# Kernel optimization log

Measured on AMD Instinct MI355X. Metric: run time of the kernel, lower is better.

## Reference

```python
import jax, jax.numpy as jnp
import numpy as np
import math

H = 16        # num heads
D = 64        # head dim
HID = 1024    # hidden size
MULT = 2      # GIN MLP multiplier
FRAC = 0.1    # top_k fraction of available predecessors
THR = 0.2     # threshold value
BASE = 10000.0  # rope base
CHUNK = 32    # query-row chunk for max aggregator
NEG = -1e30


def _rope(x, pos):
    # x: (b, H, S, D); pos: (b, S) int
    d = x.shape[-1]
    inv = 1.0 / (BASE ** (jnp.arange(0, d, 2, dtype=jnp.float32) / d))
    ang = pos.astype(jnp.float32)[..., None] * inv            # (b, S, d//2)
    cos = jnp.concatenate([jnp.cos(ang)] * 2, -1)[:, None]    # (b, 1, S, d)
    sin = jnp.concatenate([jnp.sin(ang)] * 2, -1)[:, None]
    x1, x2 = jnp.split(x, 2, axis=-1)
    return x * cos + jnp.concatenate([-x2, x1], -1) * sin


def _scaled_topk_causal(adj):
    # faithful vectorization of scaled_topk_causal_4d: per query row i, keep
    # top max(1, ceil(FRAC*i)) of the (threshold-filtered) strict predecessors.
    S = adj.shape[-1]
    j = jnp.arange(S)
    strict = j[None, :] < j[:, None]                           # (S, S) j < i
    # torch: filtered = a[:, :i] * (a >= thr)  -> below-threshold become 0
    filtered = jnp.where(strict, jnp.where(adj >= THR, adj, 0.0), NEG)
    order = jnp.argsort(-filtered, axis=-1)                    # descending, stable
    rank = jnp.argsort(order, axis=-1)                         # inverse permutation
    k = jnp.maximum(1, jnp.ceil(FRAC * jnp.arange(S, dtype=jnp.float32))).astype(jnp.int32)
    k = k.at[0].set(0)                                         # row 0 has no predecessors
    return ((rank < k[None, None, :, None]) & strict).astype(adj.dtype)


def reference(hidden_states, Wq, Wk, Wv, Wo, W1, W2, eps, position_ids):
    b, S, _ = hidden_states.shape
    q = (hidden_states @ Wq).reshape(b, S, H, D).transpose(0, 2, 1, 3)
    kk = (hidden_states @ Wk).reshape(b, S, H, D).transpose(0, 2, 1, 3)
    v = (hidden_states @ Wv).reshape(b, S, H, D).transpose(0, 2, 1, 3)
    q = _rope(q, position_ids)
    kk = _rope(kk, position_ids)
    scores = jnp.einsum('bhid,bhjd->bhij', q, kk) / math.sqrt(D)
    adj = _scaled_topk_causal(scores)                          # binary (b,H,S,S)
    deg = adj.sum(-1)                                          # (b,H,S)
    denom = jnp.maximum(deg, 1.0)[..., None]
    s_agg = jnp.einsum('bhij,bhjd->bhid', adj, v)              # sum
    m_agg = s_agg / denom                                      # mean
    var = jnp.maximum(jnp.einsum('bhij,bhjd->bhid', adj, v * v) / denom - m_agg ** 2, 0.0)
    # max aggregator: masked max over selected predecessors, chunked over rows
    nc = S // CHUNK
    adj_c = jnp.moveaxis(adj.reshape(b, H, nc, CHUNK, S), 2, 0)  # (nc,b,H,C,S)
    mx = jax.lax.map(
        lambda ac: jnp.max(jnp.where(ac[..., None] > 0, v[:, :, None, :, :], NEG), axis=-2),
        adj_c)                                                 # (nc,b,H,C,D)
    mx = jnp.moveaxis(mx, 0, 2).reshape(b, H, S, D)
    mx = jnp.where(deg[..., None] > 0, mx, 0.0)
    comb = jnp.concatenate([s_agg, m_agg, mx, var], -1)        # (b,H,S,4D)
    h1 = jax.nn.silu(jnp.einsum('bhsf,hfm->bhsm', comb, W1))   # per-head GIN MLP
    head_out = jnp.einsum('bhsm,hmd->bhsd', h1, W2) + eps * v  # epsilon-scaled residual
    return head_out.transpose(0, 2, 1, 3).reshape(b, S, H * D) @ Wo


def setup_inputs() -> dict:
    key = jax.random.key(0)
    ks = jax.random.split(key, 8)
    b, S = 1, 1024
    sc = 0.02
    return {
        'hidden_states': jax.random.normal(ks[0], (b, S, HID), jnp.float32),
        'Wq': jax.random.normal(ks[1], (HID, H * D), jnp.float32) * sc,
        'Wk': jax.random.normal(ks[2], (HID, H * D), jnp.float32) * sc,
        'Wv': jax.random.normal(ks[3], (HID, H * D), jnp.float32) * sc,
        'Wo': jax.random.normal(ks[4], (H * D, HID), jnp.float32) * sc,
        'W1': jax.random.normal(ks[5], (H, 4 * D, MULT * D), jnp.float32) * sc,
        'W2': jax.random.normal(ks[6], (H, MULT * D, D), jnp.float32) * sc,
        'eps': jnp.asarray(0.1, jnp.float32),
        'position_ids': jnp.arange(S, dtype=jnp.int32)[None, :],
    }
```

## Files before the change

### kernel.cpp

```cpp
#include <hip/hip_runtime.h>
#include <math.h>

#define NEGF  -1e30f
#define TAU   1e-6f

static __device__ __forceinline__ int imin(int a, int b) { return a < b ? a : b; }

static __device__ __forceinline__ void fma44(float A[4][4], const float4 xa, const float4 yb) {
  A[0][0] += xa.x * yb.x; A[0][1] += xa.x * yb.y; A[0][2] += xa.x * yb.z; A[0][3] += xa.x * yb.w;
  A[1][0] += xa.y * yb.x; A[1][1] += xa.y * yb.y; A[1][2] += xa.y * yb.z; A[1][3] += xa.y * yb.w;
  A[2][0] += xa.z * yb.x; A[2][1] += xa.z * yb.y; A[2][2] += xa.z * yb.z; A[2][3] += xa.z * yb.w;
  A[3][0] += xa.w * yb.x; A[3][1] += xa.w * yb.y; A[3][2] += xa.w * yb.z; A[3][3] += xa.w * yb.w;
}

static __device__ __forceinline__ void fold44(float T[4][4], float A[4][4]) {
#pragma unroll
  for (int e = 0; e < 4; ++e)
#pragma unroll
    for (int f = 0; f < 4; ++f) { T[e][f] = __fadd_rn(T[e][f], A[e][f]); A[e][f] = 0.0f; }
}

template <int MODE>
__global__ __launch_bounds__(256) void gemm64(
    const float* __restrict__ A, const float* __restrict__ B, float* __restrict__ C,
    const float* __restrict__ R, const float* __restrict__ eps_p,
    int M, int N, int K, int lda, int ldb, int ldc,
    long sA, long sB, long sC)
{
  const int z = blockIdx.z;
  A += (long)z * sA;
  B += (long)z * sB;
  float* Cf = C + (long)z * sC;
  const float* Rz = (MODE == 2) ? (R + (long)z * sC) : nullptr;

  const int bm = blockIdx.x * 64;
  const int bn = blockIdx.y * 64;
  const int tid = threadIdx.x;
  const int r0 = (tid >> 4) * 4;
  const int c0 = (tid & 15) * 4;

  __shared__ float As[16][68];
  __shared__ float Bs[16][64];

  float acc[4][4] = {};

  const int ar = tid >> 2;
  const int ac = (tid & 3) * 4;
  const int br = tid >> 4;
  const int bc = (tid & 15) * 4;

  for (int kt = 0; kt < K; kt += 16) {
    float4 av = *(const float4*)(A + (long)(bm + ar) * lda + kt + ac);
    float4 bv = *(const float4*)(B + (long)(kt + br) * ldb + bn + bc);
    As[ac + 0][ar] = av.x;
    As[ac + 1][ar] = av.y;
    As[ac + 2][ar] = av.z;
    As[ac + 3][ar] = av.w;
    *(float4*)&Bs[br][bc] = bv;
    __syncthreads();
#pragma unroll
    for (int kk = 0; kk < 16; ++kk) {
      const float4 xa = *(const float4*)&As[kk][r0];
      const float4 yb = *(const float4*)&Bs[kk][c0];
      fma44(acc, xa, yb);
    }
    __syncthreads();
  }

  const float ev = (MODE == 2) ? eps_p[0] : 0.0f;
#pragma unroll
  for (int e = 0; e < 4; ++e)
#pragma unroll
    for (int f = 0; f < 4; ++f) {
      const int r = bm + r0 + e;
      const int c = bn + c0 + f;
      float x = acc[e][f];
      if (MODE == 1) x = x / (1.0f + expf(-x));
      if (MODE == 2) x += ev * Rz[(long)r * ldc + c];
      Cf[(long)r * ldc + c] = x;
    }
}

__global__ __launch_bounds__(256) void gemm_qkv_s48(
    const float* __restrict__ A,
    const float* __restrict__ Wq, const float* __restrict__ Wk, const float* __restrict__ Wv,
    float* __restrict__ part)
{
  const int z = blockIdx.z;
  const int mat = z % 3;
  const int panel = z / 3;
  const float* B = (mat == 0) ? Wq : (mat == 1) ? Wk : Wv;
  float* P = part + ((long)(mat * 3 + panel) << 20);

  const int k0 = panel * 384;
  const int k1 = (panel == 2) ? 1024 : (k0 + 384);

  const int bm = blockIdx.x * 64;
  const int bn = blockIdx.y * 128;
  const int tid = threadIdx.x;
  const int r0 = (tid >> 4) * 4;
  const int c0 = (tid & 15) * 4;

  __shared__ float As[2][16][68];
  __shared__ float Bs[2][16][132];

  float aL[4][4] = {}, aR[4][4] = {};

  const int ar = tid >> 2;
  const int ac = (tid & 3) * 4;
  const int br = tid >> 4;
  const int bc = (tid & 15) * 4;

  {
    float4 av = *(const float4*)(A + (long)(bm + ar) * 1024 + k0 + ac);
    float4 b0 = *(const float4*)(B + (long)(k0 + br) * 1024 + bn + bc);
    float4 b1 = *(const float4*)(B + (long)(k0 + br) * 1024 + bn + bc + 64);
    As[0][ac + 0][ar] = av.x; As[0][ac + 1][ar] = av.y;
    As[0][ac + 2][ar] = av.z; As[0][ac + 3][ar] = av.w;
    *(float4*)&Bs[0][br][bc] = b0;
    *(float4*)&Bs[0][br][bc + 64] = b1;
  }
  __syncthreads();

  int cur = 0;
  for (int kt = k0; kt < k1; kt += 16) {
    const bool more = (kt + 16 < k1);
    float4 avn, b0n, b1n;
    if (more) {
      avn = *(const float4*)(A + (long)(bm + ar) * 1024 + kt + 16 + ac);
      b0n = *(const float4*)(B + (long)(kt + 16 + br) * 1024 + bn + bc);
      b1n = *(const float4*)(B + (long)(kt + 16 + br) * 1024 + bn + bc + 64);
    }
#pragma unroll
    for (int kk = 0; kk < 16; ++kk) {
      const float4 xa = *(const float4*)&As[cur][kk][r0];
      const float4 y0 = *(const float4*)&Bs[cur][kk][c0];
      const float4 y1 = *(const float4*)&Bs[cur][kk][64 + c0];
      fma44(aL, xa, y0);
      fma44(aR, xa, y1);
    }
    if (more) {
      const int nxt = cur ^ 1;
      As[nxt][ac + 0][ar] = avn.x; As[nxt][ac + 1][ar] = avn.y;
      As[nxt][ac + 2][ar] = avn.z; As[nxt][ac + 3][ar] = avn.w;
      *(float4*)&Bs[nxt][br][bc] = b0n;
      *(float4*)&Bs[nxt][br][bc + 64] = b1n;
      __syncthreads();
      cur = nxt;
    }
  }

#pragma unroll
  for (int e = 0; e < 4; ++e) {
    float* prow = P + (long)(bm + r0 + e) * 1024 + bn;
#pragma unroll
    for (int f = 0; f < 4; ++f) {
      prow[c0 + f]      = aL[e][f];
      prow[64 + c0 + f] = aR[e][f];
    }
  }
}

__global__ __launch_bounds__(256) void combine_qkv(
    const float4* __restrict__ part, float4* __restrict__ dst)
{
  const int idx = blockIdx.x * 256 + threadIdx.x;
  const int mat = idx >> 18;
  const int w = idx & 0x3FFFF;
  const long b = (long)(mat * 3) << 18;
  const float4 s0 = part[b + w];
  const float4 s1 = part[b + (1L << 18) + w];
  const float4 s2 = part[b + (2L << 18) + w];
  float4 r;
  r.x = __fadd_rn(__fadd_rn(s0.x, s1.x), s2.x);
  r.y = __fadd_rn(__fadd_rn(s0.y, s1.y), s2.y);
  r.z = __fadd_rn(__fadd_rn(s0.z, s1.z), s2.z);
  r.w = __fadd_rn(__fadd_rn(s0.w, s1.w), s2.w);
  dst[idx] = r;
}

__global__ __launch_bounds__(256) void combine_out(
    const float4* __restrict__ p, float4* __restrict__ dst)
{
  const int idx = blockIdx.x * 256 + threadIdx.x;
  const float4 a = p[idx];
  const float4 b = p[idx + (1 << 18)];
  float4 r;
  r.x = __fadd_rn(a.x, b.x);
  r.y = __fadd_rn(a.y, b.y);
  r.z = __fadd_rn(a.z, b.z);
  r.w = __fadd_rn(a.w, b.w);
  dst[idx] = r;
}

__global__ __launch_bounds__(256) void gemm_qkv64(
    const float* __restrict__ A,
    const float* __restrict__ Wq, const float* __restrict__ Wk, const float* __restrict__ Wv,
    float* __restrict__ qo, float* __restrict__ ko, float* __restrict__ vo)
{
  const int z = blockIdx.z;
  const float* B = (z == 0) ? Wq : (z == 1) ? Wk : Wv;
  float* C = (z == 0) ? qo : (z == 1) ? ko : vo;

  const int bm = blockIdx.x * 64;
  const int bn = blockIdx.y * 64;
  const int tid = threadIdx.x;
  const int r0 = (tid >> 4) * 4;
  const int c0 = (tid & 15) * 4;

  __shared__ float As[2][32][68];
  __shared__ float Bs[2][32][64];

  float acc[4][4] = {};
  float tot[4][4] = {};

  const int ar = tid >> 2;
  const int ac = (tid & 3) * 8;
  const int br = tid >> 3;
  const int bc = (tid & 7) * 8;

  {
    float4 a0 = *(const float4*)(A + (long)(bm + ar) * 1024 + ac);
    float4 a1 = *(const float4*)(A + (long)(bm + ar) * 1024 + ac + 4);
    float4 b0 = *(const float4*)(B + (long)br * 1024 + bn + bc);
    float4 b1 = *(const float4*)(B + (long)br * 1024 + bn + bc + 4);
    As[0][ac + 0][ar] = a0.x; As[0][ac + 1][ar] = a0.y;
    As[0][ac + 2][ar] = a0.z; As[0][ac + 3][ar] = a0.w;
    As[0][ac + 4][ar] = a1.x; As[0][ac + 5][ar] = a1.y;
    As[0][ac + 6][ar] = a1.z; As[0][ac + 7][ar] = a1.w;
    *(float4*)&Bs[0][br][bc] = b0;
    *(float4*)&Bs[0][br][bc + 4] = b1;
  }
  __syncthreads();

  int cur = 0;
  for (int kt = 0; kt < 1024; kt += 32) {
    const bool more = (kt + 32 < 1024);
    float4 a0n, a1n, b0n, b1n;
    if (more) {
      a0n = *(const float4*)(A + (long)(bm + ar) * 1024 + kt + 32 + ac);
      a1n = *(const float4*)(A + (long)(bm + ar) * 1024 + kt + 32 + ac + 4);
      b0n = *(const float4*)(B + (long)(kt + 32 + br) * 1024 + bn + bc);
      b1n = *(const float4*)(B + (long)(kt + 32 + br) * 1024 + bn + bc + 4);
    }
    if (kt == 384 || kt == 768) {
      fold44(tot, acc);
    }
#pragma unroll
    for (int kk = 0; kk < 32; ++kk) {
      const float4 xa = *(const float4*)&As[cur][kk][r0];
      const float4 yb = *(const float4*)&Bs[cur][kk][c0];
      fma44(acc, xa, yb);
    }
    if (more) {
      const int nxt = cur ^ 1;
      As[nxt][ac + 0][ar] = a0n.x; As[nxt][ac + 1][ar] = a0n.y;
      As[nxt][ac + 2][ar] = a0n.z; As[nxt][ac + 3][ar] = a0n.w;
      As[nxt][ac + 4][ar] = a1n.x; As[nxt][ac + 5][ar] = a1n.y;
      As[nxt][ac + 6][ar] = a1n.z; As[nxt][ac + 7][ar] = a1n.w;
      *(float4*)&Bs[nxt][br][bc] = b0n;
      *(float4*)&Bs[nxt][br][bc + 4] = b1n;
      __syncthreads();
      cur = nxt;
    }
  }

#pragma unroll
  for (int e = 0; e < 4; ++e)
#pragma unroll
    for (int f = 0; f < 4; ++f)
      C[(long)(bm + r0 + e) * 1024 + bn + c0 + f] = __fadd_rn(tot[e][f], acc[e][f]);
}

__global__ __launch_bounds__(256) void rope_table(
    const int* __restrict__ pos_ids, float2* __restrict__ tab)
{
  const int g = blockIdx.x * 256 + threadIdx.x;
  const int t = g & 31;
  const int s = g >> 5;

  const float e = (float)(2 * t) / 64.0f;
  const float p32 = (float)pow(10000.0, (double)e);
  const float inv = __fdiv_rn(1.0f, p32);
  const float posf = (float)pos_ids[s];
  const float ang = __fmul_rn(posf, inv);
  tab[g] = make_float2((float)cos((double)ang), (float)sin((double)ang));
}

__global__ __launch_bounds__(256) void rope_apply(float* __restrict__ q,
                                                  float* __restrict__ kb,
                                                  const float2* __restrict__ tab)
{
  const int g = blockIdx.x * blockDim.x + threadIdx.x;
  const int t = g & 31;
  const int h = (g >> 5) & 15;
  const int s = (g >> 9) & 1023;
  const int buf = g >> 19;
  float* p = buf ? kb : q;

  const float2 cs = tab[s * 32 + t];
  const float c  = cs.x;
  const float sn = cs.y;

  const int base = s * 1024 + h * 64;
  const float x1 = p[base + t];
  const float x2 = p[base + t + 32];
  p[base + t]      = __fadd_rn(__fmul_rn(x1, c), __fmul_rn(-x2, sn));
  p[base + t + 32] = __fadd_rn(__fmul_rn(x2, c), __fmul_rn(x1, sn));
}

__global__ __launch_bounds__(256) void gemm_score(
    const float* __restrict__ q, const float* __restrict__ kb,
    float* __restrict__ S, int headBase)
{
  const int x = blockIdx.x;
  int bmT = 0;
  while ((bmT + 1) * (bmT + 2) / 2 <= x) ++bmT;
  const int bnT = x - bmT * (bmT + 1) / 2;

  const int hl = blockIdx.y;
  const int off = (headBase + hl) * 64;
  const int bm = bmT * 64;
  const int bn = bnT * 64;
  const int tid = threadIdx.x;
  const int r0 = (tid >> 4) * 4;
  const int c0 = (tid & 15) * 4;

  __shared__ float As[16][68];
  __shared__ float Bs[16][68];

  float acc[4][4] = {};

  const int ar = tid >> 2;
  const int ac = (tid & 3) * 4;

  for (int kt = 0; kt < 64; kt += 16) {
    float4 av = *(const float4*)(q  + (long)(bm + ar) * 1024 + off + kt + ac);
    float4 bv = *(const float4*)(kb + (long)(bn + ar) * 1024 + off + kt + ac);
    As[ac + 0][ar] = av.x; As[ac + 1][ar] = av.y;
    As[ac + 2][ar] = av.z; As[ac + 3][ar] = av.w;
    Bs[ac + 0][ar] = bv.x; Bs[ac + 1][ar] = bv.y;
    Bs[ac + 2][ar] = bv.z; Bs[ac + 3][ar] = bv.w;
    __syncthreads();
#pragma unroll
    for (int kk = 0; kk < 16; ++kk) {
      const float4 xa = *(const float4*)&As[kk][r0];
      const float4 yb = *(const float4*)&Bs[kk][c0];
      fma44(acc, xa, yb);
    }
    __syncthreads();
  }

#pragma unroll
  for (int e = 0; e < 4; ++e)
#pragma unroll
    for (int f = 0; f < 4; ++f)
      S[((long)hl * 1024 + bm + r0 + e) * 1024 + bn + c0 + f] = acc[e][f] * 0.125f;
}

#define UFV(m) ((raw[m] >= 0.2f) ? __float_as_uint(raw[m]) : 0u)

__global__ __launch_bounds__(256) void select_agg5(
    const float* __restrict__ S, const float* __restrict__ v,
    float* __restrict__ comb, int headBase)
{
  const int tid = threadIdx.x;
  const int lane = tid & 63;
  const int wid = tid >> 6;
  const int i = blockIdx.x * 4 + wid;
  const int hl = blockIdx.y;
  const int h = headBase + hl;

  __shared__ int histS[4][256];
  __shared__ unsigned listS[4][128];
  int* hist = histS[wid];
  unsigned* list = listS[wid];

  const int jb = lane * 16;
  const int njc = i - jb;
  const int nj = njc < 0 ? 0 : (njc > 16 ? 16 : njc);

  const float* row = S + ((long)hl * 1024 + i) * 1024;
  float raw[16];
  {
    const float4 r0 = *(const float4*)(row + jb);
    const float4 r1 = *(const float4*)(row + jb + 4);
    const float4 r2 = *(const float4*)(row + jb + 8);
    const float4 r3 = *(const float4*)(row + jb + 12);
    raw[0]=r0.x; raw[1]=r0.y; raw[2]=r0.z; raw[3]=r0.w;
    raw[4]=r1.x; raw[5]=r1.y; raw[6]=r1.z; raw[7]=r1.w;
    raw[8]=r2.x; raw[9]=r2.y; raw[10]=r2.z; raw[11]=r2.w;
    raw[12]=r3.x; raw[13]=r3.y; raw[14]=r3.z; raw[15]=r3.w;
  }
#pragma unroll
  for (int m = 0; m < 16; ++m)
    if (m >= nj) raw[m] = 0.0f;

  const int kk = (i > 0) ? (i + 9) / 10 : 0;
  unsigned V = 0u;
  int need_eq = 0;
  unsigned fmask = 0u;

  if (kk > 0) {
    int c3E = 0, c3F = 0, cHI = 0;
    bool anyBig = false;
#pragma unroll
    for (int m = 0; m < 16; ++m) {
      const unsigned u = UFV(m);
      if (u != 0u) {
        const unsigned tb = u >> 24;
        if (tb == 0x3Eu) ++c3E;
        else if (tb == 0x3Fu) ++c3F;
        else { ++cHI; if (tb > 0x40u) anyBig = true; }
      }
    }
    const bool fastOK = (__ballot(anyBig) == 0ull);
    unsigned pk = (unsigned)c3E | ((unsigned)c3F << 10) | ((unsigned)cHI << 20);
#pragma unroll
    for (int off = 1; off < 64; off <<= 1)
      pk += (unsigned)__shfl_xor((int)pk, off, 64);
    const int t3E = (int)(pk & 1023u);
    const int t3F = (int)((pk >> 10) & 1023u);
    const int tHI = (int)((pk >> 20) & 1023u);
    const int totNZ = t3E + t3F + tHI;

    unsigned prefix = 0;
    int rk = kk;
    bool done = false;
    for (int pass = 0; pass < 4 && !done; ++pass) {
      const int shift = 24 - 8 * pass;
      if (pass == 0 && fastOK) {
        if (totNZ < rk) {
          V = 0u; need_eq = rk - totNZ; done = true;
        } else {
          int selBin, scnt;
          if (tHI >= rk)            { selBin = 0x40; scnt = tHI; }
          else if (tHI + t3F >= rk) { selBin = 0x3F; scnt = t3F; rk -= tHI; }
          else                      { selBin = 0x3E; scnt = t3E; rk -= tHI + t3F; }
          prefix = (unsigned)selBin;
          if (rk == scnt) {
            unsigned vm = 0xFFFFFFFFu;
#pragma unroll
            for (int m = 0; m < 16; ++m) {
              const unsigned u = UFV(m);
              if (u != 0u && (u >> shift) == prefix && u < vm) vm = u;
            }
#pragma unroll
            for (int off = 1; off < 64; off <<= 1) {
              const unsigned o = (unsigned)__shfl_xor((int)vm, off, 64);
              if (o < vm) vm = o;
            }
            V = vm; need_eq = 0x3FFFFFFF; done = true;
          }
        }
        continue;
      }
      *(int4*)&hist[lane * 4] = make_int4(0, 0, 0, 0);
      asm volatile("s_waitcnt lgkmcnt(0)" ::: "memory");
      __builtin_amdgcn_sched_barrier(0);
#pragma unroll
      for (int m = 0; m < 16; ++m) {
        const unsigned u = UFV(m);
        if (u != 0u && (pass == 0 || (u >> (shift + 8)) == prefix))
          atomicAdd(&hist[(u >> shift) & 0xFF], 1);
      }
      asm volatile("s_waitcnt lgkmcnt(0)" ::: "memory");
      __builtin_amdgcn_sched_barrier(0);
      const int4 hv = *(const int4*)&hist[lane * 4];
      const int s = hv.x + hv.y + hv.z + hv.w;
      int suf = s;
#pragma unroll
      for (int off = 1; off < 64; off <<= 1) {
        const int o = __shfl_down(suf, off, 64);
        if (lane + off < 64) suf += o;
      }
      const int tot = __shfl(suf, 0, 64);
      if (pass == 0 && tot < rk) {
        V = 0u; need_eq = rk - tot; done = true;
      } else {
        const int above = suf - s;
        const int sfx3 = above + hv.w;
        const int sfx2 = sfx3 + hv.z;
        const int sfx1 = sfx2 + hv.y;
        const int sfx0 = suf;
        int mbin = -1, mh = 0, msfx = 0;
        if (!(pass == 0 && lane == 0) && sfx0 >= rk && sfx0 - hv.x < rk) { mbin = lane * 4 + 0; mh = hv.x; msfx = sfx0; }
        if (sfx1 >= rk && sfx1 - hv.y < rk) { mbin = lane * 4 + 1; mh = hv.y; msfx = sfx1; }
        if (sfx2 >= rk && sfx2 - hv.z < rk) { mbin = lane * 4 + 2; mh = hv.z; msfx = sfx2; }
        if (sfx3 >= rk && sfx3 - hv.w < rk) { mbin = lane * 4 + 3; mh = hv.w; msfx = sfx3; }
        const unsigned long long bal = __ballot(mbin >= 0);
        const int src = (int)__ffsll((unsigned long long)bal) - 1;
        const int selBin = __shfl(mbin, src, 64) & 0xFF;
        const int scnt = __shfl(mh, src, 64);
        const int ssfx = __shfl(msfx, src, 64);
        prefix = (prefix << 8) | (unsigned)selBin;
        rk = rk - (ssfx - scnt);
        if (rk == scnt) {
          unsigned vm = 0xFFFFFFFFu;
#pragma unroll
          for (int m = 0; m < 16; ++m) {
            const unsigned u = UFV(m);
            if (u != 0u && (u >> shift) == prefix && u < vm) vm = u;
          }
#pragma unroll
          for (int off = 1; off < 64; off <<= 1) {
            const unsigned o = (unsigned)__shfl_xor((int)vm, off, 64);
            if (o < vm) vm = o;
          }
          V = vm; need_eq = 0x3FFFFFFF; done = true;
        }
      }
    }
    if (!done) { V = prefix; need_eq = rk; }

    int e = 0;
#pragma unroll
    for (int m = 0; m < 16; ++m) if (m < nj && UFV(m) == V) ++e;
    int val = e;
#pragma unroll
    for (int off = 1; off < 64; off <<= 1) {
      const int n = __shfl_up(val, off, 64);
      if (lane >= off) val += n;
    }
    int excl = val - e;
#pragma unroll
    for (int m = 0; m < 16; ++m) if (m < nj) {
      const unsigned u = UFV(m);
      if (u > V) fmask |= (1u << m);
      else if (u == V) { if (excl < need_eq) fmask |= (1u << m); ++excl; }
    }
  }

  int hypOut = -1, hypIn = -1;
  if (kk > 0 && kk < i) {
    unsigned wmax = 0u;
    int mIn = -1;
    unsigned long long tbIn = ~0ull, tbOut = ~0ull;
#pragma unroll
    for (int m = 0; m < 16; ++m) if (m < nj) {
      const int j = jb + m;
      const unsigned u = UFV(m);
      if ((fmask >> m) & 1u) {
        if (u == V && j > mIn) mIn = j;
        const float fv = __uint_as_float(u);
        const float dd = fv - 0.2f;
        if (fv >= 0.2f && dd < TAU) {
          const unsigned long long p = (((unsigned long long)__float_as_uint(dd)) << 32) | (unsigned)j;
          if (p < tbIn) tbIn = p;
        }
      } else {
        if (u > wmax) wmax = u;
        if (raw[m] < 0.2f) {
          const float dd = 0.2f - raw[m];
          if (dd < TAU) {
            const unsigned long long p = (((unsigned long long)__float_as_uint(dd)) << 32) | (unsigned)j;
            if (p < tbOut) tbOut = p;
          }
        }
      }
    }
#pragma unroll
    for (int off = 1; off < 64; off <<= 1) {
      const unsigned ow = (unsigned)__shfl_xor((int)wmax, off, 64);
      if (ow > wmax) wmax = ow;
      const int om = __shfl_xor(mIn, off, 64);
      if (om > mIn) mIn = om;
      const unsigned long long oi = __shfl_xor(tbIn, off, 64);
      if (oi < tbIn) tbIn = oi;
      const unsigned long long oo = __shfl_xor(tbOut, off, 64);
      if (oo < tbOut) tbOut = oo;
    }
    int outMin = 0x7FFFFFFF;
#pragma unroll
    for (int m = 0; m < 16; ++m) if (m < nj) {
      if (!((fmask >> m) & 1u) && UFV(m) == wmax) {
        const int j = jb + m;
        if (j < outMin) outMin = j;
      }
    }
#pragma unroll
    for (int off = 1; off < 64; off <<= 1) {
      const int o = __shfl_xor(outMin, off, 64);
      if (o < outMin) outMin = o;
    }
    float bestD = TAU;
    int oI = -1, nI = -1;
    if (outMin != 0x7FFFFFFF && mIn >= 0) {
      const float Vf = __uint_as_float(V);
      const float Wf = __uint_as_float(wmax);
      if (!(wmax == V && V == 0u)) {
        const float gapA = Vf - Wf;
        if (gapA < bestD) { bestD = gapA; oI = mIn; nI = outMin; }
      }
      if (tbIn != ~0ull) {
        const float d = __uint_as_float((unsigned)(tbIn >> 32));
        const int jj = (int)(tbIn & 0xFFFFFFFFu);
        const bool noop = (wmax == 0u && jj < outMin);
        if (!noop && d < bestD) { bestD = d; oI = jj; nI = outMin; }
      }
      if (tbOut != ~0ull && Vf <= 0.2f) {
        const float d = __uint_as_float((unsigned)(tbOut >> 32));
        const int jj = (int)(tbOut & 0xFFFFFFFFu);
        if (d < bestD) { bestD = d; oI = mIn; nI = jj; }
      }
    }
    hypOut = oI; hypIn = nI;
  }

  const bool amb = (hypOut >= 0);
  unsigned smask = 0u;
  int cnt = 0;
#pragma unroll
  for (int m = 0; m < 16; ++m) if (m < nj) {
    const int j = jb + m;
    int s1 = (int)((fmask >> m) & 1u);
    if (amb) { if (j == hypOut) s1 = 0; if (j == hypIn) s1 = 1; }
    if (s1) smask |= (1u << m);
    if (((fmask >> m) & 1u) | (unsigned)s1) ++cnt;
  }
  int val2 = cnt;
#pragma unroll
  for (int off = 1; off < 64; off <<= 1) {
    const int n = __shfl_up(val2, off, 64);
    if (lane >= off) val2 += n;
  }
  const int L = __shfl(val2, 63, 64);
  int base = val2 - cnt;
#pragma unroll
  for (int m = 0; m < 16; ++m) if (m < nj) {
    const unsigned f0b = (fmask >> m) & 1u;
    const unsigned s1b = (smask >> m) & 1u;
    if (f0b | s1b) {
      list[base] = (unsigned)(jb + m) | (f0b << 10) | (s1b << 11);
      ++base;
    }
  }
  asm volatile("s_waitcnt lgkmcnt(0)" ::: "memory");
  __builtin_amdgcn_sched_barrier(0);

  const float denom = (float)(kk > 0 ? kk : 1);
  const float* vcol = v + h * 64 + lane;
  float* crow = comb + ((long)(h * 1024 + i)) * 256;

  if (!amb) {
    float sum0 = 0, sq0 = 0, mx0 = NEGF;
    for (int e2 = 0; e2 < L; e2 += 4) {
      const uint4 en4 = *(const uint4*)&list[e2];
      float v0 = 0, v1 = 0, v2 = 0, v3 = 0;
      const bool b0 = (e2 + 0 < L), b1 = (e2 + 1 < L), b2 = (e2 + 2 < L), b3 = (e2 + 3 < L);
      if (b0) v0 = vcol[(long)(en4.x & 1023) * 1024];
      if (b1) v1 = vcol[(long)(en4.y & 1023) * 1024];
      if (b2) v2 = vcol[(long)(en4.z & 1023) * 1024];
      if (b3) v3 = vcol[(long)(en4.w & 1023) * 1024];
      if (b0) { sum0 += v0; sq0 += v0 * v0; mx0 = fmaxf(mx0, v0); }
      if (b1) { sum0 += v1; sq0 += v1 * v1; mx0 = fmaxf(mx0, v1); }
      if (b2) { sum0 += v2; sq0 += v2 * v2; mx0 = fmaxf(mx0, v2); }
      if (b3) { sum0 += v3; sq0 += v3 * v3; mx0 = fmaxf(mx0, v3); }
    }
    const float mean0 = sum0 / denom;
    const float var0 = fmaxf(sq0 / denom - mean0 * mean0, 0.0f);
    const float mx0o = (kk > 0) ? mx0 : 0.0f;
    crow[lane]       = sum0;
    crow[64 + lane]  = mean0;
    crow[128 + lane] = mx0o;
    crow[192 + lane] = var0;
  } else {
    float sum0 = 0, sq0 = 0, mx0 = NEGF, sum1 = 0, sq1 = 0, mx1 = NEGF;
    for (int e2 = 0; e2 < L; e2 += 4) {
      const uint4 en4 = *(const uint4*)&list[e2];
      const unsigned w0 = (e2 + 0 < L) ? en4.x : 0u;
      const unsigned w1 = (e2 + 1 < L) ? en4.y : 0u;
      const unsigned w2 = (e2 + 2 < L) ? en4.z : 0u;
      const unsigned w3 = (e2 + 3 < L) ? en4.w : 0u;
      float v0 = 0, v1 = 0, v2 = 0, v3 = 0;
      if (w0) v0 = vcol[(long)(w0 & 1023) * 1024];
      if (w1) v1 = vcol[(long)(w1 & 1023) * 1024];
      if (w2) v2 = vcol[(long)(w2 & 1023) * 1024];
      if (w3) v3 = vcol[(long)(w3 & 1023) * 1024];
      if (w0 & (1u << 10)) { sum0 += v0; sq0 += v0 * v0; mx0 = fmaxf(mx0, v0); }
      if (w0 & (1u << 11)) { sum1 += v0; sq1 += v0 * v0; mx1 = fmaxf(mx1, v0); }
      if (w1 & (1u << 10)) { sum0 += v1; sq0 += v1 * v1; mx0 = fmaxf(mx0, v1); }
      if (w1 & (1u << 11)) { sum1 += v1; sq1 += v1 * v1; mx1 = fmaxf(mx1, v1); }
      if (w2 & (1u << 10)) { sum0 += v2; sq0 += v2 * v2; mx0 = fmaxf(mx0, v2); }
      if (w2 & (1u << 11)) { sum1 += v2; sq1 += v2 * v2; mx1 = fmaxf(mx1, v2); }
      if (w3 & (1u << 10)) { sum0 += v3; sq0 += v3 * v3; mx0 = fmaxf(mx0, v3); }
      if (w3 & (1u << 11)) { sum1 += v3; sq1 += v3 * v3; mx1 = fmaxf(mx1, v3); }
    }
    const float mean0 = sum0 / denom, mean1 = sum1 / denom;
    const float var0 = fmaxf(sq0 / denom - mean0 * mean0, 0.0f);
    const float var1 = fmaxf(sq1 / denom - mean1 * mean1, 0.0f);
    const float mx0o = (kk > 0) ? mx0 : 0.0f;
    const float mx1o = (kk > 0) ? mx1 : 0.0f;
    crow[lane]       = 0.5f * (sum0 + sum1);
    crow[64 + lane]  = 0.5f * (mean0 + mean1);
    crow[128 + lane] = 0.5f * (mx0o + mx1o);
    crow[192 + lane] = 0.5f * (var0 + var1);
  }
}

extern "C" void kernel_launch(void* const* d_in, const int* in_sizes, int n_in,
                              void* d_out, int out_size, void* d_ws, size_t ws_size,
                              hipStream_t stream)
{
  const float* hidden = (const float*)d_in[0];
  const float* Wq = (const float*)d_in[1];
  const float* Wk = (const float*)d_in[2];
  const float* Wv = (const float*)d_in[3];
  const float* Wo = (const float*)d_in[4];
  const float* W1 = (const float*)d_in[5];
  const float* W2 = (const float*)d_in[6];
  const float* eps = (const float*)d_in[7];
  const int* pos = (const int*)d_in[8];

  const size_t MB = 1024UL * 1024UL;
  int G = 4;
  if (ws_size >= 28 * MB + 64 * MB) G = 16;
  else if (ws_size >= 28 * MB + 32 * MB) G = 8;

  float* q      = (float*)d_ws;
  float* kbuf   = q + (1 << 20);
  float* v      = kbuf + (1 << 20);
  float* comb   = v + (1 << 20);
  float* scores = comb + (1 << 22);
  float* h1     = scores;
  float* ho     = scores + (1 << 21);
  float2* tab   = (float2*)comb;
  float* parts  = comb;

  const dim3 blk(256);

  if (ws_size >= 64 * MB) {
    float* part = scores;
    gemm_qkv_s48<<<dim3(16, 8, 9), blk, 0, stream>>>(hidden, Wq, Wk, Wv, part);
    combine_qkv<<<dim3(3072), blk, 0, stream>>>((const float4*)part, (float4*)q);
  } else {
    gemm_qkv64<<<dim3(16, 16, 3), blk, 0, stream>>>(hidden, Wq, Wk, Wv, q, kbuf, v);
  }

  rope_table<<<128, blk, 0, stream>>>(pos, tab);
  rope_apply<<<4096, blk, 0, stream>>>(q, kbuf, tab);

  for (int g = 0; g < 16; g += G) {
    gemm_score<<<dim3(136, G), blk, 0, stream>>>(q, kbuf, scores, g);
    select_agg5<<<dim3(256, G), blk, 0, stream>>>(scores, v, comb, g);
  }

  gemm64<1><<<dim3(16, 2, 16), blk, 0, stream>>>(comb, W1, h1, nullptr, nullptr,
      1024, 128, 256, 256, 128, 128, (long)1024 * 256, (long)256 * 128, (long)1024 * 128);

  gemm64<2><<<dim3(16, 1, 16), blk, 0, stream>>>(h1, W2, ho, v, eps,
      1024, 64, 128, 128, 64, 1024, (long)1024 * 128, (long)128 * 64, 64);

  gemm64<0><<<dim3(16, 16, 2), blk, 0, stream>>>(ho, Wo, parts, nullptr, nullptr,
      1024, 1024, 512, 1024, 1024, 1024, 512, (long)512 * 1024, (long)1 << 20);
  combine_out<<<dim3(1024), blk, 0, stream>>>((const float4*)parts, (float4*)d_out);
}
```

Baseline: 337.9 us.

## Fuse QKV split-K combine with RoPE and widen causal score tiles

```diff
diff --git a/kernel.cpp b/kernel.cpp
--- a/kernel.cpp
+++ b/kernel.cpp
@@ -161,22 +161,63 @@
   }
 }
 
-__global__ __launch_bounds__(256) void combine_qkv(
-    const float4* __restrict__ part, float4* __restrict__ dst)
-{
-  const int idx = blockIdx.x * 256 + threadIdx.x;
-  const int mat = idx >> 18;
-  const int w = idx & 0x3FFFF;
-  const long b = (long)(mat * 3) << 18;
-  const float4 s0 = part[b + w];
-  const float4 s1 = part[b + (1L << 18) + w];
-  const float4 s2 = part[b + (2L << 18) + w];
-  float4 r;
-  r.x = __fadd_rn(__fadd_rn(s0.x, s1.x), s2.x);
-  r.y = __fadd_rn(__fadd_rn(s0.y, s1.y), s2.y);
-  r.z = __fadd_rn(__fadd_rn(s0.z, s1.z), s2.z);
-  r.w = __fadd_rn(__fadd_rn(s0.w, s1.w), s2.w);
-  dst[idx] = r;
+__global__ __launch_bounds__(256) void combine_rope(
+    const float4* __restrict__ part, const float2* __restrict__ tab,
+    float4* __restrict__ q, float4* __restrict__ k, float4* __restrict__ v)
+{
+  const int g = blockIdx.x * 256 + threadIdx.x;
+  if (g < 262144) {
+    const int buf = g >> 17;
+    const int rem = g & 131071;
+    const int s   = rem >> 7;
+    const int hx  = (rem >> 3) & 15;
+    const int t4  = rem & 7;
+    const int w   = s * 256 + hx * 16 + t4;
+    const long b  = (long)(buf * 3) << 18;
+
+    const float4 a0 = part[b + w];
+    const float4 a1 = part[b + (1L << 18) + w];
+    const float4 a2 = part[b + (2L << 18) + w];
+    const float4 c0 = part[b + w + 8];
+    const float4 c1 = part[b + (1L << 18) + w + 8];
+    const float4 c2 = part[b + (2L << 18) + w + 8];
+
+    float lo[4], hi[4];
+    lo[0] = __fadd_rn(__fadd_rn(a0.x, a1.x), a2.x);
+    lo[1] = __fadd_rn(__fadd_rn(a0.y, a1.y), a2.y);
+    lo[2] = __fadd_rn(__fadd_rn(a0.z, a1.z), a2.z);
+    lo[3] = __fadd_rn(__fadd_rn(a0.w, a1.w), a2.w);
+    hi[0] = __fadd_rn(__fadd_rn(c0.x, c1.x), c2.x);
+    hi[1] = __fadd_rn(__fadd_rn(c0.y, c1.y), c2.y);
+    hi[2] = __fadd_rn(__fadd_rn(c0.z, c1.z), c2.z);
+    hi[3] = __fadd_rn(__fadd_rn(c0.w, c1.w), c2.w);
+
+    float ol[4], oh[4];
+#pragma unroll
+    for (int c = 0; c < 4; ++c) {
+      const int t = t4 * 4 + c;
+      const float2 cs = tab[s * 32 + t];
+      const float x1 = lo[c];
+      const float x2 = hi[c];
+      ol[c] = __fadd_rn(__fmul_rn(x1, cs.x), __fmul_rn(-x2, cs.y));
+      oh[c] = __fadd_rn(__fmul_rn(x2, cs.x), __fmul_rn(x1, cs.y));
+    }
+    float4* dst = buf ? k : q;
+    dst[w]     = make_float4(ol[0], ol[1], ol[2], ol[3]);
+    dst[w + 8] = make_float4(oh[0], oh[1], oh[2], oh[3]);
+  } else {
+    const int w = g - 262144;
+    const long b = (long)6 << 18;
+    const float4 s0 = part[b + w];
+    const float4 s1 = part[b + (1L << 18) + w];
+    const float4 s2 = part[b + (2L << 18) + w];
+    float4 r;
+    r.x = __fadd_rn(__fadd_rn(s0.x, s1.x), s2.x);
+    r.y = __fadd_rn(__fadd_rn(s0.y, s1.y), s2.y);
+    r.z = __fadd_rn(__fadd_rn(s0.z, s1.z), s2.z);
+    r.w = __fadd_rn(__fadd_rn(s0.w, s1.w), s2.w);
+    v[w] = r;
+  }
 }
 
 __global__ __launch_bounds__(256) void combine_out(
@@ -309,53 +350,97 @@
   p[base + t + 32] = __fadd_rn(__fmul_rn(x2, c), __fmul_rn(x1, sn));
 }
 
-__global__ __launch_bounds__(256) void gemm_score(
+__global__ __launch_bounds__(256) void gemm_score128(
     const float* __restrict__ q, const float* __restrict__ kb,
     float* __restrict__ S, int headBase)
 {
   const int x = blockIdx.x;
-  int bmT = 0;
-  while ((bmT + 1) * (bmT + 2) / 2 <= x) ++bmT;
-  const int bnT = x - bmT * (bmT + 1) / 2;
+  int R = 0, accum = 0;
+  while (accum + ((R + 2) >> 1) <= x) { accum += (R + 2) >> 1; ++R; }
+  const int b = x - accum;
+  const bool wide = (2 * b + 1 <= R);
 
   const int hl = blockIdx.y;
   const int off = (headBase + hl) * 64;
-  const int bm = bmT * 64;
-  const int bn = bnT * 64;
+  const int bm = R * 64;
+  const int bn = 128 * b;
   const int tid = threadIdx.x;
   const int r0 = (tid >> 4) * 4;
   const int c0 = (tid & 15) * 4;
 
-  __shared__ float As[16][68];
-  __shared__ float Bs[16][68];
-
-  float acc[4][4] = {};
+  __shared__ float As[2][16][68];
+  __shared__ float Bs[2][16][132];
+
+  float aL[4][4] = {}, aR[4][4] = {};
 
   const int ar = tid >> 2;
   const int ac = (tid & 3) * 4;
-
+  const int r2 = wide ? (bn + 64 + ar) : (bn + ar);
+
+  {
+    const float4 qa = *(const float4*)(q  + (long)(bm + ar) * 1024 + off + ac);
+    const float4 ka = *(const float4*)(kb + (long)(bn + ar) * 1024 + off + ac);
+    const float4 kc = *(const float4*)(kb + (long)r2 * 1024 + off + ac);
+    As[0][ac + 0][ar] = qa.x; As[0][ac + 1][ar] = qa.y;
+    As[0][ac + 2][ar] = qa.z; As[0][ac + 3][ar] = qa.w;
+    Bs[0][ac + 0][ar] = ka.x; Bs[0][ac + 1][ar] = ka.y;
+    Bs[0][ac + 2][ar] = ka.z; Bs[0][ac + 3][ar] = ka.w;
+    Bs[0][ac + 0][64 + ar] = kc.x; Bs[0][ac + 1][64 + ar] = kc.y;
+    Bs[0][ac + 2][64 + ar] = kc.z; Bs[0][ac + 3][64 + ar] = kc.w;
+  }
+  __syncthreads();
+
+  int cur = 0;
   for (int kt = 0; kt < 64; kt += 16) {
-    float4 av = *(const float4*)(q  + (long)(bm + ar) * 1024 + off + kt + ac);
-    float4 bv = *(const float4*)(kb + (long)(bn + ar) * 1024 + off + kt + ac);
-    As[ac + 0][ar] = av.x; As[ac + 1][ar] = av.y;
-    As[ac + 2][ar] = av.z; As[ac + 3][ar] = av.w;
-    Bs[ac + 0][ar] = bv.x; Bs[ac + 1][ar] = bv.y;
-    Bs[ac + 2][ar] = bv.z; Bs[ac + 3][ar] = bv.w;
-    __syncthreads();
-#pragma unroll
-    for (int kk = 0; kk < 16; ++kk) {
-      const float4 xa = *(const float4*)&As[kk][r0];
-      const float4 yb = *(const float4*)&Bs[kk][c0];
-      fma44(acc, xa, yb);
-    }
-    __syncthreads();
-  }
-
-#pragma unroll
-  for (int e = 0; e < 4; ++e)
+    const bool more = (kt + 16 < 64);
+    float4 qan, kan, kcn;
+    if (more) {
+      qan = *(const float4*)(q  + (long)(bm + ar) * 1024 + off + kt + 16 + ac);
+      kan = *(const float4*)(kb + (long)(bn + ar) * 1024 + off + kt + 16 + ac);
+      kcn = *(const float4*)(kb + (long)r2 * 1024 + off + kt + 16 + ac);
+    }
+    if (wide) {
+#pragma unroll
+      for (int kk = 0; kk < 16; ++kk) {
+        const float4 xa = *(const float4*)&As[cur][kk][r0];
+        const float4 y0 = *(const float4*)&Bs[cur][kk][c0];
+        const float4 y1 = *(const float4*)&Bs[cur][kk][64 + c0];
+        fma44(aL, xa, y0);
+        fma44(aR, xa, y1);
+      }
+    } else {
+#pragma unroll
+      for (int kk = 0; kk < 16; ++kk) {
+        const float4 xa = *(const float4*)&As[cur][kk][r0];
+        const float4 y0 = *(const float4*)&Bs[cur][kk][c0];
+        fma44(aL, xa, y0);
+      }
+    }
+    if (more) {
+      const int nxt = cur ^ 1;
+      As[nxt][ac + 0][ar] = qan.x; As[nxt][ac + 1][ar] = qan.y;
+      As[nxt][ac + 2][ar] = qan.z; As[nxt][ac + 3][ar] = qan.w;
+      Bs[nxt][ac + 0][ar] = kan.x; Bs[nxt][ac + 1][ar] = kan.y;
+      Bs[nxt][ac + 2][ar] = kan.z; Bs[nxt][ac + 3][ar] = kan.w;
+      Bs[nxt][ac + 0][64 + ar] = kcn.x; Bs[nxt][ac + 1][64 + ar] = kcn.y;
+      Bs[nxt][ac + 2][64 + ar] = kcn.z; Bs[nxt][ac + 3][64 + ar] = kcn.w;
+      __syncthreads();
+      cur = nxt;
+    }
+  }
+
+#pragma unroll
+  for (int e = 0; e < 4; ++e) {
+    float* srow = S + ((long)hl * 1024 + bm + r0 + e) * 1024 + bn;
 #pragma unroll
     for (int f = 0; f < 4; ++f)
-      S[((long)hl * 1024 + bm + r0 + e) * 1024 + bn + c0 + f] = acc[e][f] * 0.125f;
+      srow[c0 + f] = aL[e][f] * 0.125f;
+    if (wide) {
+#pragma unroll
+      for (int f = 0; f < 4; ++f)
+        srow[64 + c0 + f] = aR[e][f] * 0.125f;
+    }
+  }
 }
 
 #define UFV(m) ((raw[m] >= 0.2f) ? __float_as_uint(raw[m]) : 0u)
@@ -729,19 +814,20 @@
 
   const dim3 blk(256);
 
+  rope_table<<<128, blk, 0, stream>>>(pos, tab);
+
   if (ws_size >= 64 * MB) {
     float* part = scores;
     gemm_qkv_s48<<<dim3(16, 8, 9), blk, 0, stream>>>(hidden, Wq, Wk, Wv, part);
-    combine_qkv<<<dim3(3072), blk, 0, stream>>>((const float4*)part, (float4*)q);
+    combine_rope<<<2048, blk, 0, stream>>>((const float4*)part, tab,
+                                           (float4*)q, (float4*)kbuf, (float4*)v);
   } else {
     gemm_qkv64<<<dim3(16, 16, 3), blk, 0, stream>>>(hidden, Wq, Wk, Wv, q, kbuf, v);
-  }
-
-  rope_table<<<128, blk, 0, stream>>>(pos, tab);
-  rope_apply<<<4096, blk, 0, stream>>>(q, kbuf, tab);
+    rope_apply<<<4096, blk, 0, stream>>>(q, kbuf, tab);
+  }
 
   for (int g = 0; g < 16; g += G) {
-    gemm_score<<<dim3(136, G), blk, 0, stream>>>(q, kbuf, scores, g);
+    gemm_score128<<<dim3(72, G), blk, 0, stream>>>(q, kbuf, scores, g);
     select_agg5<<<dim3(256, G), blk, 0, stream>>>(scores, v, comb, g);
   }
 
```

After: 342.6 us. About the same (+1.4%).

## Fuse QKV split-K combine with RoPE; stripe select rows across lanes with ballots

Applied to the files above, without the earlier changes.

```diff
diff --git a/kernel.cpp b/kernel.cpp
--- a/kernel.cpp
+++ b/kernel.cpp
@@ -161,22 +161,63 @@
   }
 }
 
-__global__ __launch_bounds__(256) void combine_qkv(
-    const float4* __restrict__ part, float4* __restrict__ dst)
-{
-  const int idx = blockIdx.x * 256 + threadIdx.x;
-  const int mat = idx >> 18;
-  const int w = idx & 0x3FFFF;
-  const long b = (long)(mat * 3) << 18;
-  const float4 s0 = part[b + w];
-  const float4 s1 = part[b + (1L << 18) + w];
-  const float4 s2 = part[b + (2L << 18) + w];
-  float4 r;
-  r.x = __fadd_rn(__fadd_rn(s0.x, s1.x), s2.x);
-  r.y = __fadd_rn(__fadd_rn(s0.y, s1.y), s2.y);
-  r.z = __fadd_rn(__fadd_rn(s0.z, s1.z), s2.z);
-  r.w = __fadd_rn(__fadd_rn(s0.w, s1.w), s2.w);
-  dst[idx] = r;
+__global__ __launch_bounds__(256) void combine_rope(
+    const float4* __restrict__ part, const float2* __restrict__ tab,
+    float4* __restrict__ q, float4* __restrict__ k, float4* __restrict__ v)
+{
+  const int g = blockIdx.x * 256 + threadIdx.x;
+  if (g < 262144) {
+    const int buf = g >> 17;
+    const int rem = g & 131071;
+    const int s   = rem >> 7;
+    const int hx  = (rem >> 3) & 15;
+    const int t4  = rem & 7;
+    const int w   = s * 256 + hx * 16 + t4;
+    const long b  = (long)(buf * 3) << 18;
+
+    const float4 a0 = part[b + w];
+    const float4 a1 = part[b + (1L << 18) + w];
+    const float4 a2 = part[b + (2L << 18) + w];
+    const float4 c0 = part[b + w + 8];
+    const float4 c1 = part[b + (1L << 18) + w + 8];
+    const float4 c2 = part[b + (2L << 18) + w + 8];
+
+    float lo[4], hi[4];
+    lo[0] = __fadd_rn(__fadd_rn(a0.x, a1.x), a2.x);
+    lo[1] = __fadd_rn(__fadd_rn(a0.y, a1.y), a2.y);
+    lo[2] = __fadd_rn(__fadd_rn(a0.z, a1.z), a2.z);
+    lo[3] = __fadd_rn(__fadd_rn(a0.w, a1.w), a2.w);
+    hi[0] = __fadd_rn(__fadd_rn(c0.x, c1.x), c2.x);
+    hi[1] = __fadd_rn(__fadd_rn(c0.y, c1.y), c2.y);
+    hi[2] = __fadd_rn(__fadd_rn(c0.z, c1.z), c2.z);
+    hi[3] = __fadd_rn(__fadd_rn(c0.w, c1.w), c2.w);
+
+    float ol[4], oh[4];
+#pragma unroll
+    for (int c = 0; c < 4; ++c) {
+      const int t = t4 * 4 + c;
+      const float2 cs = tab[s * 32 + t];
+      const float x1 = lo[c];
+      const float x2 = hi[c];
+      ol[c] = __fadd_rn(__fmul_rn(x1, cs.x), __fmul_rn(-x2, cs.y));
+      oh[c] = __fadd_rn(__fmul_rn(x2, cs.x), __fmul_rn(x1, cs.y));
+    }
+    float4* dst = buf ? k : q;
+    dst[w]     = make_float4(ol[0], ol[1], ol[2], ol[3]);
+    dst[w + 8] = make_float4(oh[0], oh[1], oh[2], oh[3]);
+  } else {
+    const int w = g - 262144;
+    const long b = (long)6 << 18;
+    const float4 s0 = part[b + w];
+    const float4 s1 = part[b + (1L << 18) + w];
+    const float4 s2 = part[b + (2L << 18) + w];
+    float4 r;
+    r.x = __fadd_rn(__fadd_rn(s0.x, s1.x), s2.x);
+    r.y = __fadd_rn(__fadd_rn(s0.y, s1.y), s2.y);
+    r.z = __fadd_rn(__fadd_rn(s0.z, s1.z), s2.z);
+    r.w = __fadd_rn(__fadd_rn(s0.w, s1.w), s2.w);
+    v[w] = r;
+  }
 }
 
 __global__ __launch_bounds__(256) void combine_out(
@@ -360,7 +401,7 @@
 
 #define UFV(m) ((raw[m] >= 0.2f) ? __float_as_uint(raw[m]) : 0u)
 
-__global__ __launch_bounds__(256) void select_agg5(
+__global__ __launch_bounds__(256) void select_agg6(
     const float* __restrict__ S, const float* __restrict__ v,
     float* __restrict__ comb, int headBase)
 {
@@ -376,25 +417,20 @@
   int* hist = histS[wid];
   unsigned* list = listS[wid];
 
-  const int jb = lane * 16;
-  const int njc = i - jb;
-  const int nj = njc < 0 ? 0 : (njc > 16 ? 16 : njc);
+  const int nlayer = (i + 63) >> 6;
+  const unsigned long long ltm = (1ull << lane) - 1ull;
 
   const float* row = S + ((long)hl * 1024 + i) * 1024;
   float raw[16];
-  {
-    const float4 r0 = *(const float4*)(row + jb);
-    const float4 r1 = *(const float4*)(row + jb + 4);
-    const float4 r2 = *(const float4*)(row + jb + 8);
-    const float4 r3 = *(const float4*)(row + jb + 12);
-    raw[0]=r0.x; raw[1]=r0.y; raw[2]=r0.z; raw[3]=r0.w;
-    raw[4]=r1.x; raw[5]=r1.y; raw[6]=r1.z; raw[7]=r1.w;
-    raw[8]=r2.x; raw[9]=r2.y; raw[10]=r2.z; raw[11]=r2.w;
-    raw[12]=r3.x; raw[13]=r3.y; raw[14]=r3.z; raw[15]=r3.w;
-  }
-#pragma unroll
-  for (int m = 0; m < 16; ++m)
-    if (m >= nj) raw[m] = 0.0f;
+#pragma unroll
+  for (int m = 0; m < 16; ++m) raw[m] = 0.0f;
+#pragma unroll
+  for (int m = 0; m < 16; ++m) {
+    if (m < nlayer) {
+      const int j = m * 64 + lane;
+      if (j < i) raw[m] = row[j];
+    }
+  }
 
   const int kk = (i > 0) ? (i + 9) / 10 : 0;
   unsigned V = 0u;
@@ -406,12 +442,14 @@
     bool anyBig = false;
 #pragma unroll
     for (int m = 0; m < 16; ++m) {
-      const unsigned u = UFV(m);
-      if (u != 0u) {
-        const unsigned tb = u >> 24;
-        if (tb == 0x3Eu) ++c3E;
-        else if (tb == 0x3Fu) ++c3F;
-        else { ++cHI; if (tb > 0x40u) anyBig = true; }
+      if (m < nlayer) {
+        const unsigned u = UFV(m);
+        if (u != 0u) {
+          const unsigned tb = u >> 24;
+          if (tb == 0x3Eu) ++c3E;
+          else if (tb == 0x3Fu) ++c3F;
+          else { ++cHI; if (tb > 0x40u) anyBig = true; }
+        }
       }
     }
     const bool fastOK = (__ballot(anyBig) == 0ull);
@@ -442,8 +480,10 @@
             unsigned vm = 0xFFFFFFFFu;
 #pragma unroll
             for (int m = 0; m < 16; ++m) {
-              const unsigned u = UFV(m);
-              if (u != 0u && (u >> shift) == prefix && u < vm) vm = u;
+              if (m < nlayer) {
+                const unsigned u = UFV(m);
+                if (u != 0u && (u >> shift) == prefix && u < vm) vm = u;
+              }
             }
 #pragma unroll
             for (int off = 1; off < 64; off <<= 1) {
@@ -460,9 +500,11 @@
       __builtin_amdgcn_sched_barrier(0);
 #pragma unroll
       for (int m = 0; m < 16; ++m) {
-        const unsigned u = UFV(m);
-        if (u != 0u && (pass == 0 || (u >> (shift + 8)) == prefix))
-          atomicAdd(&hist[(u >> shift) & 0xFF], 1);
+        if (m < nlayer) {
+          const unsigned u = UFV(m);
+          if (u != 0u && (pass == 0 || (u >> (shift + 8)) == prefix))
+            atomicAdd(&hist[(u >> shift) & 0xFF], 1);
+        }
       }
       asm volatile("s_waitcnt lgkmcnt(0)" ::: "memory");
       __builtin_amdgcn_sched_barrier(0);
@@ -499,8 +541,10 @@
           unsigned vm = 0xFFFFFFFFu;
 #pragma unroll
           for (int m = 0; m < 16; ++m) {
-            const unsigned u = UFV(m);
-            if (u != 0u && (u >> shift) == prefix && u < vm) vm = u;
+            if (m < nlayer) {
+              const unsigned u = UFV(m);
+              if (u != 0u && (u >> shift) == prefix && u < vm) vm = u;
+            }
           }
 #pragma unroll
           for (int off = 1; off < 64; off <<= 1) {
@@ -513,21 +557,24 @@
     }
     if (!done) { V = prefix; need_eq = rk; }
 
-    int e = 0;
-#pragma unroll
-    for (int m = 0; m < 16; ++m) if (m < nj && UFV(m) == V) ++e;
-    int val = e;
-#pragma unroll
-    for (int off = 1; off < 64; off <<= 1) {
-      const int n = __shfl_up(val, off, 64);
-      if (lane >= off) val += n;
-    }
-    int excl = val - e;
-#pragma unroll
-    for (int m = 0; m < 16; ++m) if (m < nj) {
-      const unsigned u = UFV(m);
-      if (u > V) fmask |= (1u << m);
-      else if (u == V) { if (excl < need_eq) fmask |= (1u << m); ++excl; }
+    int prefEq = 0;
+#pragma unroll
+    for (int m = 0; m < 16; ++m) {
+      if (m < nlayer) {
+        const int j = m * 64 + lane;
+        const bool validm = (j < i);
+        const unsigned u = UFV(m);
+        const bool eq = validm && (u == V);
+        const unsigned long long bal = __ballot(eq);
+        if (validm) {
+          if (u > V) fmask |= (1u << m);
+          else if (eq) {
+            const int excl = prefEq + __popcll(bal & ltm);
+            if (excl < need_eq) fmask |= (1u << m);
+          }
+        }
+        prefEq += (int)__popcll(bal);
+      }
     }
   }
 
@@ -537,24 +584,28 @@
     int mIn = -1;
     unsigned long long tbIn = ~0ull, tbOut = ~0ull;
 #pragma unroll
-    for (int m = 0; m < 16; ++m) if (m < nj) {
-      const int j = jb + m;
-      const unsigned u = UFV(m);
-      if ((fmask >> m) & 1u) {
-        if (u == V && j > mIn) mIn = j;
-        const float fv = __uint_as_float(u);
-        const float dd = fv - 0.2f;
-        if (fv >= 0.2f && dd < TAU) {
-          const unsigned long long p = (((unsigned long long)__float_as_uint(dd)) << 32) | (unsigned)j;
-          if (p < tbIn) tbIn = p;
-        }
-      } else {
-        if (u > wmax) wmax = u;
-        if (raw[m] < 0.2f) {
-          const float dd = 0.2f - raw[m];
-          if (dd < TAU) {
-            const unsigned long long p = (((unsigned long long)__float_as_uint(dd)) << 32) | (unsigned)j;
-            if (p < tbOut) tbOut = p;
+    for (int m = 0; m < 16; ++m) {
+      if (m < nlayer) {
+        const int j = m * 64 + lane;
+        if (j < i) {
+          const unsigned u = UFV(m);
+          if ((fmask >> m) & 1u) {
+            if (u == V && j > mIn) mIn = j;
+            const float fv = __uint_as_float(u);
+            const float dd = fv - 0.2f;
+            if (fv >= 0.2f && dd < TAU) {
+              const unsigned long long p = (((unsigned long long)__float_as_uint(dd)) << 32) | (unsigned)j;
+              if (p < tbIn) tbIn = p;
+            }
+          } else {
+            if (u > wmax) wmax = u;
+            if (raw[m] < 0.2f) {
+              const float dd = 0.2f - raw[m];
+              if (dd < TAU) {
+                const unsigned long long p = (((unsigned long long)__float_as_uint(dd)) << 32) | (unsigned)j;
+                if (p < tbOut) tbOut = p;
+              }
+            }
           }
         }
       }
@@ -572,10 +623,12 @@
     }
     int outMin = 0x7FFFFFFF;
 #pragma unroll
-    for (int m = 0; m < 16; ++m) if (m < nj) {
-      if (!((fmask >> m) & 1u) && UFV(m) == wmax) {
-        const int j = jb + m;
-        if (j < outMin) outMin = j;
+    for (int m = 0; m < 16; ++m) {
+      if (m < nlayer) {
+        const int j = m * 64 + lane;
+        if (j < i && !((fmask >> m) & 1u) && UFV(m) == wmax) {
+          if (j < outMin) outMin = j;
+        }
       }
     }
 #pragma unroll
@@ -608,33 +661,25 @@
   }
 
   const bool amb = (hypOut >= 0);
-  unsigned smask = 0u;
-  int cnt = 0;
-#pragma unroll
-  for (int m = 0; m < 16; ++m) if (m < nj) {
-    const int j = jb + m;
-    int s1 = (int)((fmask >> m) & 1u);
-    if (amb) { if (j == hypOut) s1 = 0; if (j == hypIn) s1 = 1; }
-    if (s1) smask |= (1u << m);
-    if (((fmask >> m) & 1u) | (unsigned)s1) ++cnt;
-  }
-  int val2 = cnt;
-#pragma unroll
-  for (int off = 1; off < 64; off <<= 1) {
-    const int n = __shfl_up(val2, off, 64);
-    if (lane >= off) val2 += n;
-  }
-  const int L = __shfl(val2, 63, 64);
-  int base = val2 - cnt;
-#pragma unroll
-  for (int m = 0; m < 16; ++m) if (m < nj) {
-    const unsigned f0b = (fmask >> m) & 1u;
-    const unsigned s1b = (smask >> m) & 1u;
-    if (f0b | s1b) {
-      list[base] = (unsigned)(jb + m) | (f0b << 10) | (s1b << 11);
-      ++base;
-    }
-  }
+  int base = 0;
+#pragma unroll
+  for (int m = 0; m < 16; ++m) {
+    if (m < nlayer) {
+      const int j = m * 64 + lane;
+      const bool validm = (j < i);
+      const unsigned f0b = (fmask >> m) & 1u;
+      int s1 = (int)f0b;
+      if (amb) { if (j == hypOut) s1 = 0; if (j == hypIn) s1 = 1; }
+      const bool sel = validm && ((f0b | (unsigned)s1) != 0u);
+      const unsigned long long bal = __ballot(sel);
+      if (sel) {
+        const int pos = base + (int)__popcll(bal & ltm);
+        list[pos] = (unsigned)j | (f0b << 10) | ((unsigned)s1 << 11);
+      }
+      base += (int)__popcll(bal);
+    }
+  }
+  const int L = base;
   asm volatile("s_waitcnt lgkmcnt(0)" ::: "memory");
   __builtin_amdgcn_sched_barrier(0);
 
@@ -729,20 +774,21 @@
 
   const dim3 blk(256);
 
+  rope_table<<<128, blk, 0, stream>>>(pos, tab);
+
   if (ws_size >= 64 * MB) {
     float* part = scores;
     gemm_qkv_s48<<<dim3(16, 8, 9), blk, 0, stream>>>(hidden, Wq, Wk, Wv, part);
-    combine_qkv<<<dim3(3072), blk, 0, stream>>>((const float4*)part, (float4*)q);
+    combine_rope<<<2048, blk, 0, stream>>>((const float4*)part, tab,
+                                           (float4*)q, (float4*)kbuf, (float4*)v);
   } else {
     gemm_qkv64<<<dim3(16, 16, 3), blk, 0, stream>>>(hidden, Wq, Wk, Wv, q, kbuf, v);
-  }
-
-  rope_table<<<128, blk, 0, stream>>>(pos, tab);
-  rope_apply<<<4096, blk, 0, stream>>>(q, kbuf, tab);
+    rope_apply<<<4096, blk, 0, stream>>>(q, kbuf, tab);
+  }
 
   for (int g = 0; g < 16; g += G) {
     gemm_score<<<dim3(136, G), blk, 0, stream>>>(q, kbuf, scores, g);
-    select_agg5<<<dim3(256, G), blk, 0, stream>>>(scores, v, comb, g);
+    select_agg6<<<dim3(256, G), blk, 0, stream>>>(scores, v, comb, g);
   }
 
   gemm64<1><<<dim3(16, 2, 16), blk, 0, stream>>>(comb, W1, h1, nullptr, nullptr,
```

Result: no change. 333.2 us (median of 3 runs) (-1.4%).
